# Kernel tuning notes

Measured on AMD Instinct MI355X. Metric: run time of the kernel, lower is better.

Reference implementation:

```python
import jax, jax.numpy as jnp
import numpy as np

V_EN = 50000; V_FR = 50000; D = 256; B = 64; S = 64; NEG = 8192; PAD = 0


def setup_inputs() -> dict:
    key = jax.random.key(0)
    k = jax.random.split(key, 8)
    zs = jax.random.normal(k[0], (B, S, D), dtype=jnp.float32) * 0.1
    x_en = jax.random.randint(k[1], (B, S), 1, V_EN)  # avoid pad row 0
    x_fr = jax.random.randint(k[2], (B, S), 1, V_FR)
    en_mask = jnp.ones((B, S), dtype=jnp.float32)
    fr_mask = jnp.ones((B, S), dtype=jnp.float32)
    W_en = jax.random.normal(k[3], (V_EN, D), dtype=jnp.float32) * 0.05
    W_en = W_en.at[PAD].set(0.0)  # padding_idx row is zero
    W_fr = jax.random.normal(k[4], (V_FR, D), dtype=jnp.float32) * 0.05
    W_fr = W_fr.at[PAD].set(0.0)
    # Host-side CSS sampling, mirroring the torch module's numpy/multinomial step.
    rng = np.random.default_rng(0)
    pos_en = np.unique(np.asarray(x_en))
    neg_en = rng.choice(np.setdiff1d(np.arange(V_EN), pos_en), NEG, replace=False)
    kappa_en = jnp.float32((V_EN - pos_en.shape[0]) / NEG)
    pos_fr = np.unique(np.asarray(x_fr))
    neg_fr = rng.choice(np.setdiff1d(np.arange(V_FR), pos_fr), NEG, replace=False)
    kappa_fr = jnp.float32((V_FR - pos_fr.shape[0]) / NEG)
    return {
        "zs": zs, "x_en": x_en, "x_fr": x_fr,
        "en_mask": en_mask, "fr_mask": fr_mask,
        "W_en": W_en, "W_fr": W_fr,
        "pos_en": jnp.asarray(pos_en), "neg_en": jnp.asarray(neg_en),
        "pos_fr": jnp.asarray(pos_fr), "neg_fr": jnp.asarray(neg_fr),
        "kappa_en": kappa_en, "kappa_fr": kappa_fr,
    }


def _css_denom(zs, W, pos_idx, neg_idx, kappa):
    # zs: [B,S,D]; pos/neg embeddings: [P,D]/[N,D] -> denom [B,S]
    pos_e = W[pos_idx]
    neg_e = W[neg_idx]
    pos_score = jnp.exp(jnp.einsum("bsd,pd->bsp", zs, pos_e)).sum(-1)
    neg_score = kappa * jnp.exp(jnp.einsum("bsd,nd->bsn", zs, neg_e)).sum(-1)
    return pos_score + neg_score


def reference(zs, x_en, x_fr, en_mask, fr_mask, W_en, W_fr,
              pos_en, neg_en, pos_fr, neg_fr, kappa_en, kappa_fr):
    # --- English CSS: per-token score ---
    be_en = W_en[x_en]                                   # [B,S,D]
    en_batch = jnp.exp((zs * be_en).sum(-1))             # [B,S]
    en_probs = en_batch / _css_denom(zs, W_en, pos_en, neg_en, kappa_en)
    # --- French CSS: alignment score against every en position ---
    be_fr = W_fr[x_fr]                                   # [B,Sf,D]
    fr_batch = jnp.exp(jnp.einsum("bfd,bsd->bfs", be_fr, zs))  # [B,Sf,S]
    fr_denom = _css_denom(zs, W_fr, pos_fr, neg_fr, kappa_fr)  # [B,S]
    fr_probs = fr_batch / fr_denom[:, None, :]
    en_rec_loss = (jnp.log(en_probs) * en_mask).sum(axis=1)            # [B]
    fr_rec_loss = (jnp.log(fr_probs.sum(axis=2)) * fr_mask).sum(axis=1)  # [B]
    return en_rec_loss, fr_rec_loss
```

## Files before the change

### kernel.cpp

```cpp
#include <hip/hip_runtime.h>

#define DDIM 256
#define NTOK 4096
#define NEGN 8192
#define TM 64
#define TN 64
#define LDT 40

typedef __attribute__((ext_vector_type(8))) short bf16x8;
typedef __attribute__((ext_vector_type(4))) float f32x4;

__device__ inline unsigned short f2bf(float f) {
    unsigned int u = __float_as_uint(f);
    unsigned int r = u + 0x7FFFu + ((u >> 16) & 1u);
    return (unsigned short)(r >> 16);
}

__device__ inline void gl_lds16(const unsigned short* g, unsigned short* l) {
    __builtin_amdgcn_global_load_lds(
        reinterpret_cast<__attribute__((address_space(1))) unsigned int*>(
            reinterpret_cast<uintptr_t>(g)),
        reinterpret_cast<__attribute__((address_space(3))) unsigned int*>(
            reinterpret_cast<uintptr_t>(l)),
        16, 0, 0);
}

__device__ inline void wait_vmcnt2() { asm volatile("s_waitcnt vmcnt(2)" ::: "memory"); }
__device__ inline void wait_vmcnt1() { asm volatile("s_waitcnt vmcnt(1)" ::: "memory"); }
__device__ inline void wait_vmcnt0() { asm volatile("s_waitcnt vmcnt(0)" ::: "memory"); }
__device__ inline void raw_barrier() { asm volatile("s_barrier" ::: "memory"); }

template<int CTRL>
__device__ inline float dpp_add(float x) {
    int v = __builtin_amdgcn_update_dpp(0, __float_as_int(x), CTRL, 0xF, 0xF, false);
    return x + __int_as_float(v);
}
__device__ inline float red16(float x) {
    x = dpp_add<0xB1>(x);
    x = dpp_add<0x4E>(x);
    x = dpp_add<0x141>(x);
    x = dpp_add<0x140>(x);
    return x;
}

__global__ void gather_kernel(
    const float* __restrict__ zs,
    const float* __restrict__ W_en, const float* __restrict__ W_fr,
    const int* __restrict__ pos_en, const int* __restrict__ neg_en,
    const int* __restrict__ pos_fr, const int* __restrict__ neg_fr,
    const int* __restrict__ x_en,
    unsigned short* __restrict__ z_bf,
    unsigned short* __restrict__ E_en, unsigned short* __restrict__ E_fr,
    float* __restrict__ en_score,
    float* __restrict__ denom_en, float* __restrict__ denom_fr,
    int Pe, int Pf, int Lpe, int Lpf)
{
    int row  = blockIdx.x * 4 + (threadIdx.x >> 6);
    int lane = threadIdx.x & 63;
    const float* src = nullptr;
    unsigned short* dst = nullptr;
    bool zero = false;

    if (row < NTOK) {
        src = zs + (size_t)row * DDIM;
        dst = z_bf + (size_t)row * DDIM;
        if (lane == 0) { denom_en[row] = 0.0f; denom_fr[row] = 0.0f; }
    } else if (row < NTOK + Lpe) {
        int j = row - NTOK;
        int Le = Pe + NEGN;
        int idx = 0;
        if (j < Pe)      idx = pos_en[j];
        else if (j < Le) idx = neg_en[j - Pe];
        else             zero = true;
        src = W_en + (size_t)idx * DDIM;
        dst = E_en + (size_t)j * DDIM;
    } else if (row < NTOK + Lpe + Lpf) {
        int j = row - NTOK - Lpe;
        int Lf = Pf + NEGN;
        int idx = 0;
        if (j < Pf)      idx = pos_fr[j];
        else if (j < Lf) idx = neg_fr[j - Pf];
        else             zero = true;
        src = W_fr + (size_t)idx * DDIM;
        dst = E_fr + (size_t)j * DDIM;
    } else if (row < NTOK + Lpe + Lpf + NTOK) {
        int j = row - NTOK - Lpe - Lpf;
        int idx = x_en[j];
        float4 z = *(const float4*)(zs   + (size_t)j   * DDIM + lane * 4);
        float4 w = *(const float4*)(W_en + (size_t)idx * DDIM + lane * 4);
        float s = z.x * w.x + z.y * w.y + z.z * w.z + z.w * w.w;
        #pragma unroll
        for (int m = 32; m; m >>= 1) s += __shfl_xor(s, m);
        if (lane == 0) en_score[j] = s;
        return;
    } else {
        return;
    }

    int d = lane * 4;
    float4 v;
    if (zero) { v.x = v.y = v.z = v.w = 0.0f; }
    else      { v = *(const float4*)(src + d); }
    ushort4 o;
    o.x = f2bf(v.x); o.y = f2bf(v.y); o.z = f2bf(v.z); o.w = f2bf(v.w);
    *(ushort4*)(dst + d) = o;
}

__global__ __launch_bounds__(256, 2) void expsum_stream(
    const unsigned short* __restrict__ A,
    const unsigned short* __restrict__ E,
    const float* __restrict__ kep, const float* __restrict__ kfp,
    float* __restrict__ out_en, float* __restrict__ out_fr,
    int Pe, int Pf, int Lpe, int NT)
{
    __shared__ __align__(16) unsigned short Bs[4][2048];

    int lin = blockIdx.y * 64 + blockIdx.x;
    int xcd = lin & 7;
    int xb  = (lin >> 3) & 15;
    int sl  = xcd + 8 * (lin >> 7);

    int t    = threadIdx.x;
    int lane = t & 63;
    int wave = t >> 6;
    int col  = lane & 15;
    int quad = lane >> 4;

    float ke = kep[0], kf = kfp[0];
    asm volatile("" : "+v"(ke), "+v"(kf) : : "memory");

    bf16x8 afr[4][8];
    {
        const unsigned short* Ap =
            A + ((size_t)(xb * 256 + wave * 64 + col)) * DDIM + quad * 8;
        #pragma unroll
        for (int i = 0; i < 4; i++)
            #pragma unroll
            for (int c = 0; c < 8; c++)
                afr[i][c] = *(const bf16x8*)(Ap + (size_t)i * 16 * DDIM + c * 32);
    }

    float sums[4][4];
    #pragma unroll
    for (int i = 0; i < 4; i++)
        #pragma unroll
        for (int rr = 0; rr < 4; rr++) sums[i][rr] = 0.0f;
    float* curout = out_en;
    int outrow = xb * 256 + wave * 64;

    int ntiles = (NT - sl + 31) >> 5;
    int C = ntiles * 8;

    #define STAGE(c) do {                                                     \
        int tl_ = sl + (((c) >> 3) << 5);                                     \
        int kk_ = ((c) & 7) * 32;                                             \
        const unsigned short* g_ =                                            \
            E + (size_t)(tl_ * 64 + wave * 16 + col) * DDIM + kk_ + quad * 8; \
        gl_lds16(g_, &Bs[(c) & 3][wave * 512]);                               \
    } while (0)

    STAGE(0);
    STAGE(1);

    for (int s = 0; s < ntiles; s++) {
        int tl = sl + (s << 5);
        int nb = tl * 64;

        float* o = (nb >= Lpe) ? out_fr : out_en;
        if (o != curout) {
            #pragma unroll
            for (int i = 0; i < 4; i++)
                #pragma unroll
                for (int rr = 0; rr < 4; rr++) {
                    float v = red16(sums[i][rr]);
                    if (col == 0)
                        atomicAdd(curout + outrow + 16 * i + quad * 4 + rr, v);
                    sums[i][rr] = 0.0f;
                }
            curout = o;
        }

        float wj[4];
        #pragma unroll
        for (int j = 0; j < 4; j++) {
            int ngl = nb + 16 * j + col;
            if (nb < Lpe) {
                wj[j] = (ngl < Pe) ? 1.0f : ((ngl < Pe + NEGN) ? ke : 0.0f);
            } else {
                int nl = ngl - Lpe;
                wj[j] = (nl < Pf) ? 1.0f : ((nl < Pf + NEGN) ? kf : 0.0f);
            }
        }

        f32x4 acc[4][4];
        #pragma unroll
        for (int i = 0; i < 4; i++)
            #pragma unroll
            for (int j = 0; j < 4; j++)
                acc[i][j] = (f32x4){0.f, 0.f, 0.f, 0.f};

        #pragma unroll
        for (int k8 = 0; k8 < 8; k8++) {
            int c  = s * 8 + k8;
            int rb = c & 3;
            if (c + 2 < C) {
                STAGE(c + 2);
                wait_vmcnt2();
            } else if (c + 1 < C) {
                wait_vmcnt1();
            } else {
                wait_vmcnt0();
            }
            raw_barrier();

            bf16x8 bfv[4];
            #pragma unroll
            for (int j = 0; j < 4; j++)
                bfv[j] = *(const bf16x8*)(&Bs[rb][j * 512 + quad * 128 + col * 8]);
            #pragma unroll
            for (int j = 0; j < 4; j++)
                #pragma unroll
                for (int i = 0; i < 4; i++)
                    acc[i][j] = __builtin_amdgcn_mfma_f32_16x16x32_bf16(
                        afr[i][k8], bfv[j], acc[i][j], 0, 0, 0);
        }

        #pragma unroll
        for (int i = 0; i < 4; i++)
            #pragma unroll
            for (int rr = 0; rr < 4; rr++) {
                sums[i][rr] += wj[0] * __expf(acc[i][0][rr])
                             + wj[1] * __expf(acc[i][1][rr])
                             + wj[2] * __expf(acc[i][2][rr])
                             + wj[3] * __expf(acc[i][3][rr]);
            }
    }
    #undef STAGE

    #pragma unroll
    for (int i = 0; i < 4; i++)
        #pragma unroll
        for (int rr = 0; rr < 4; rr++) {
            float v = red16(sums[i][rr]);
            if (col == 0)
                atomicAdd(curout + outrow + 16 * i + quad * 4 + rr, v);
        }
}

__global__ __launch_bounds__(256) void expsum_gemm64_loss(
    const float* __restrict__ W_fr,
    const int* __restrict__ x_fr,
    const unsigned short* __restrict__ Bm,
    const float* __restrict__ denom_fr,
    const float* __restrict__ denom_en,
    const float* __restrict__ en_score,
    const float* __restrict__ en_mask,
    const float* __restrict__ fr_mask,
    float* __restrict__ outloss)
{
    __shared__ __align__(16) unsigned short lda[TM * LDT];
    __shared__ __align__(16) unsigned short ldb[TN * LDT];
    __shared__ float tbuf[64];

    int batch = blockIdx.x;
    const unsigned short* Bb = Bm + (size_t)batch * TN * DDIM;

    int t      = threadIdx.x;
    int srow   = t >> 2;
    int schunk = t & 3;
    int lane   = t & 63;
    int wave   = t >> 6;
    int col    = lane & 15;
    int quad   = lane >> 4;

    int aidx = x_fr[batch * 64 + srow];
    const float* Arow = W_fr + (size_t)aidx * DDIM;

    f32x4 acc0 = {0.f,0.f,0.f,0.f};
    f32x4 acc1 = {0.f,0.f,0.f,0.f};
    f32x4 acc2 = {0.f,0.f,0.f,0.f};
    f32x4 acc3 = {0.f,0.f,0.f,0.f};

    for (int kk = 0; kk < DDIM; kk += 32) {
        float4 f0 = *(const float4*)(Arow + kk + schunk * 8);
        float4 f1 = *(const float4*)(Arow + kk + schunk * 8 + 4);
        uint4 bv = *(const uint4*)(Bb + (size_t)srow * DDIM + kk + schunk * 8);
        ushort4 ua; ua.x = f2bf(f0.x); ua.y = f2bf(f0.y); ua.z = f2bf(f0.z); ua.w = f2bf(f0.w);
        ushort4 ub; ub.x = f2bf(f1.x); ub.y = f2bf(f1.y); ub.z = f2bf(f1.z); ub.w = f2bf(f1.w);
        __syncthreads();
        *(ushort4*)(lda + srow * LDT + schunk * 8)     = ua;
        *(ushort4*)(lda + srow * LDT + schunk * 8 + 4) = ub;
        *(uint4*)(ldb + srow * LDT + schunk * 8) = bv;
        __syncthreads();

        bf16x8 af = *(const bf16x8*)(lda + (wave * 16 + col) * LDT + quad * 8);
        bf16x8 b0 = *(const bf16x8*)(ldb + ( 0 + col) * LDT + quad * 8);
        bf16x8 b1 = *(const bf16x8*)(ldb + (16 + col) * LDT + quad * 8);
        bf16x8 b2 = *(const bf16x8*)(ldb + (32 + col) * LDT + quad * 8);
        bf16x8 b3 = *(const bf16x8*)(ldb + (48 + col) * LDT + quad * 8);
        acc0 = __builtin_amdgcn_mfma_f32_16x16x32_bf16(af, b0, acc0, 0, 0, 0);
        acc1 = __builtin_amdgcn_mfma_f32_16x16x32_bf16(af, b1, acc1, 0, 0, 0);
        acc2 = __builtin_amdgcn_mfma_f32_16x16x32_bf16(af, b2, acc2, 0, 0, 0);
        acc3 = __builtin_amdgcn_mfma_f32_16x16x32_bf16(af, b3, acc3, 0, 0, 0);
    }

    const float* db = denom_fr + batch * 64;
    float w0 = 1.0f / db[ 0 + col];
    float w1 = 1.0f / db[16 + col];
    float w2 = 1.0f / db[32 + col];
    float w3 = 1.0f / db[48 + col];

    float tot0 = w0 * __expf(acc0.x) + w1 * __expf(acc1.x) + w2 * __expf(acc2.x) + w3 * __expf(acc3.x);
    float tot1 = w0 * __expf(acc0.y) + w1 * __expf(acc1.y) + w2 * __expf(acc2.y) + w3 * __expf(acc3.y);
    float tot2 = w0 * __expf(acc0.z) + w1 * __expf(acc1.z) + w2 * __expf(acc2.z) + w3 * __expf(acc3.z);
    float tot3 = w0 * __expf(acc0.w) + w1 * __expf(acc1.w) + w2 * __expf(acc2.w) + w3 * __expf(acc3.w);

    #pragma unroll
    for (int m = 1; m < 16; m <<= 1) {
        tot0 += __shfl_xor(tot0, m);
        tot1 += __shfl_xor(tot1, m);
        tot2 += __shfl_xor(tot2, m);
        tot3 += __shfl_xor(tot3, m);
    }
    if (col == 0) {
        int base = wave * 16 + quad * 4;
        tbuf[base + 0] = tot0; tbuf[base + 1] = tot1;
        tbuf[base + 2] = tot2; tbuf[base + 3] = tot3;
    }
    __syncthreads();

    if (t < 64) {
        int i = batch * 64 + t;
        float a = (en_score[i] - __logf(denom_en[i])) * en_mask[i];
        float c = __logf(tbuf[t]) * fr_mask[i];
        #pragma unroll
        for (int m = 32; m; m >>= 1) { a += __shfl_xor(a, m); c += __shfl_xor(c, m); }
        if (t == 0) { outloss[batch] = a; outloss[64 + batch] = c; }
    }
}

extern "C" void kernel_launch(void* const* d_in, const int* in_sizes, int n_in,
                              void* d_out, int out_size, void* d_ws, size_t ws_size,
                              hipStream_t stream)
{
    const float* zs       = (const float*)d_in[0];
    const int*   x_en     = (const int*)d_in[1];
    const int*   x_fr     = (const int*)d_in[2];
    const float* en_mask  = (const float*)d_in[3];
    const float* fr_mask  = (const float*)d_in[4];
    const float* W_en     = (const float*)d_in[5];
    const float* W_fr     = (const float*)d_in[6];
    const int*   pos_en   = (const int*)d_in[7];
    const int*   neg_en   = (const int*)d_in[8];
    const int*   pos_fr   = (const int*)d_in[9];
    const int*   neg_fr   = (const int*)d_in[10];
    const float* kappa_en = (const float*)d_in[11];
    const float* kappa_fr = (const float*)d_in[12];

    int Pe  = in_sizes[7];
    int Pf  = in_sizes[9];
    int Lpe = (Pe + NEGN + 63) & ~63;
    int Lpf = (Pf + NEGN + 63) & ~63;
    int Ltot = Lpe + Lpf;
    int NT   = Ltot / 64;

    char* w = (char*)d_ws;
    float* denom_en = (float*)w; w += NTOK * 4;
    float* denom_fr = (float*)w; w += NTOK * 4;
    float* en_score = (float*)w; w += NTOK * 4;
    unsigned short* z_bf  = (unsigned short*)w; w += (size_t)NTOK * DDIM * 2;
    unsigned short* E_all = (unsigned short*)w; w += (size_t)Ltot * DDIM * 2;

    int totrows = NTOK + Lpe + Lpf + NTOK;
    gather_kernel<<<(totrows + 3) / 4, 256, 0, stream>>>(
        zs, W_en, W_fr, pos_en, neg_en, pos_fr, neg_fr, x_en,
        z_bf, E_all, E_all + (size_t)Lpe * DDIM,
        en_score, denom_en, denom_fr, Pe, Pf, Lpe, Lpf);

    expsum_stream<<<dim3(64, 8), 256, 0, stream>>>(
        z_bf, E_all, kappa_en, kappa_fr, denom_en, denom_fr, Pe, Pf, Lpe, NT);

    expsum_gemm64_loss<<<64, 256, 0, stream>>>(
        W_fr, x_fr, z_bf, denom_fr, denom_en, en_score, en_mask, fr_mask,
        (float*)d_out);
}
```

Before: 202.2 us.

## Split expsum stream into single-wave blocks with barrier-free triple-buffered prefetch

The streaming exp-sum GEMM now runs as 2048 blocks of one 64-lane wave, where it used to be 512 blocks of four waves sharing each LDS tile. Each wave loads the full 64-row embedding tile into LDS on its own, so the workgroup s_barrier is gone. Prefetch depth rises from two to three stages, with vmcnt waits adjusted to match. The cost is that waves no longer share E tiles, so each tile is fetched once per 64-row token group rather than once per 256-row group, roughly quadrupling L2/LDS fill traffic for E.

```diff
diff --git a/kernel.cpp b/kernel.cpp
--- a/kernel.cpp
+++ b/kernel.cpp
@@ -25,10 +25,9 @@
         16, 0, 0);
 }
 
-__device__ inline void wait_vmcnt2() { asm volatile("s_waitcnt vmcnt(2)" ::: "memory"); }
-__device__ inline void wait_vmcnt1() { asm volatile("s_waitcnt vmcnt(1)" ::: "memory"); }
+__device__ inline void wait_vmcnt8() { asm volatile("s_waitcnt vmcnt(8)" ::: "memory"); }
+__device__ inline void wait_vmcnt4() { asm volatile("s_waitcnt vmcnt(4)" ::: "memory"); }
 __device__ inline void wait_vmcnt0() { asm volatile("s_waitcnt vmcnt(0)" ::: "memory"); }
-__device__ inline void raw_barrier() { asm volatile("s_barrier" ::: "memory"); }
 
 template<int CTRL>
 __device__ inline float dpp_add(float x) {
@@ -106,7 +105,7 @@
     *(ushort4*)(dst + d) = o;
 }
 
-__global__ __launch_bounds__(256, 2) void expsum_stream(
+__global__ __launch_bounds__(64, 2) void expsum_stream(
     const unsigned short* __restrict__ A,
     const unsigned short* __restrict__ E,
     const float* __restrict__ kep, const float* __restrict__ kfp,
@@ -115,14 +114,12 @@
 {
     __shared__ __align__(16) unsigned short Bs[4][2048];
 
-    int lin = blockIdx.y * 64 + blockIdx.x;
+    int lin = blockIdx.x;
     int xcd = lin & 7;
-    int xb  = (lin >> 3) & 15;
-    int sl  = xcd + 8 * (lin >> 7);
-
-    int t    = threadIdx.x;
-    int lane = t & 63;
-    int wave = t >> 6;
+    int sl  = xcd + 8 * ((lin >> 3) & 3);
+    int mg  = lin >> 5;
+
+    int lane = threadIdx.x;
     int col  = lane & 15;
     int quad = lane >> 4;
 
@@ -131,8 +128,7 @@
 
     bf16x8 afr[4][8];
     {
-        const unsigned short* Ap =
-            A + ((size_t)(xb * 256 + wave * 64 + col)) * DDIM + quad * 8;
+        const unsigned short* Ap = A + ((size_t)(mg * 64 + col)) * DDIM + quad * 8;
         #pragma unroll
         for (int i = 0; i < 4; i++)
             #pragma unroll
@@ -146,7 +142,7 @@
         #pragma unroll
         for (int rr = 0; rr < 4; rr++) sums[i][rr] = 0.0f;
     float* curout = out_en;
-    int outrow = xb * 256 + wave * 64;
+    int outrow = mg * 64;
 
     int ntiles = (NT - sl + 31) >> 5;
     int C = ntiles * 8;
@@ -155,12 +151,17 @@
         int tl_ = sl + (((c) >> 3) << 5);                                     \
         int kk_ = ((c) & 7) * 32;                                             \
         const unsigned short* g_ =                                            \
-            E + (size_t)(tl_ * 64 + wave * 16 + col) * DDIM + kk_ + quad * 8; \
-        gl_lds16(g_, &Bs[(c) & 3][wave * 512]);                               \
+            E + (size_t)(tl_ * 64 + col) * DDIM + kk_ + quad * 8;             \
+        unsigned short* l_ = &Bs[(c) & 3][0];                                 \
+        gl_lds16(g_,             l_);                                         \
+        gl_lds16(g_ + 16 * DDIM, l_ + 512);                                   \
+        gl_lds16(g_ + 32 * DDIM, l_ + 1024);                                  \
+        gl_lds16(g_ + 48 * DDIM, l_ + 1536);                                  \
     } while (0)
 
     STAGE(0);
     STAGE(1);
+    STAGE(2);
 
     for (int s = 0; s < ntiles; s++) {
         int tl = sl + (s << 5);
@@ -201,22 +202,22 @@
 
         #pragma unroll
         for (int k8 = 0; k8 < 8; k8++) {
-            int c  = s * 8 + k8;
-            int rb = c & 3;
+            int c = s * 8 + k8;
             if (c + 2 < C) {
-                STAGE(c + 2);
-                wait_vmcnt2();
+                wait_vmcnt8();
             } else if (c + 1 < C) {
-                wait_vmcnt1();
+                wait_vmcnt4();
             } else {
                 wait_vmcnt0();
             }
-            raw_barrier();
 
             bf16x8 bfv[4];
             #pragma unroll
             for (int j = 0; j < 4; j++)
-                bfv[j] = *(const bf16x8*)(&Bs[rb][j * 512 + quad * 128 + col * 8]);
+                bfv[j] = *(const bf16x8*)(&Bs[c & 3][j * 512 + quad * 128 + col * 8]);
+
+            if (c + 3 < C) STAGE(c + 3);
+
             #pragma unroll
             for (int j = 0; j < 4; j++)
                 #pragma unroll
@@ -377,7 +378,7 @@
         z_bf, E_all, E_all + (size_t)Lpe * DDIM,
         en_score, denom_en, denom_fr, Pe, Pf, Lpe, Lpf);
 
-    expsum_stream<<<dim3(64, 8), 256, 0, stream>>>(
+    expsum_stream<<<2048, 64, 0, stream>>>(
         z_bf, E_all, kappa_en, kappa_fr, denom_en, denom_fr, Pe, Pf, Lpe, NT);
 
     expsum_gemm64_loss<<<64, 256, 0, stream>>>(
```

Result: slower. 246.5 us (+21.9%).

## Double-buffer whole E tiles in LDS with one barrier per tile

Applied to the files above, without the earlier changes.

Replaces the per-k-chunk four-slot ring buffer with a two-tile double buffer that prefetches all eight k-chunks of the next tile at once. Each tile now needs a single wait and barrier instead of eight, cutting synchronisation overhead and lengthening the prefetch distance. LDS use per block grows fourfold, which could limit occupancy. The full drain at the start of each tile may expose memory latency if the previous tile's compute does not cover it.

```diff
diff --git a/kernel.cpp b/kernel.cpp
--- a/kernel.cpp
+++ b/kernel.cpp
@@ -25,8 +25,6 @@
         16, 0, 0);
 }
 
-__device__ inline void wait_vmcnt2() { asm volatile("s_waitcnt vmcnt(2)" ::: "memory"); }
-__device__ inline void wait_vmcnt1() { asm volatile("s_waitcnt vmcnt(1)" ::: "memory"); }
 __device__ inline void wait_vmcnt0() { asm volatile("s_waitcnt vmcnt(0)" ::: "memory"); }
 __device__ inline void raw_barrier() { asm volatile("s_barrier" ::: "memory"); }
 
@@ -113,7 +111,7 @@
     float* __restrict__ out_en, float* __restrict__ out_fr,
     int Pe, int Pf, int Lpe, int NT)
 {
-    __shared__ __align__(16) unsigned short Bs[4][2048];
+    __shared__ __align__(16) unsigned short Bs[2][8][2048];
 
     int lin = blockIdx.y * 64 + blockIdx.x;
     int xcd = lin & 7;
@@ -149,22 +147,27 @@
     int outrow = xb * 256 + wave * 64;
 
     int ntiles = (NT - sl + 31) >> 5;
-    int C = ntiles * 8;
-
-    #define STAGE(c) do {                                                     \
-        int tl_ = sl + (((c) >> 3) << 5);                                     \
-        int kk_ = ((c) & 7) * 32;                                             \
-        const unsigned short* g_ =                                            \
-            E + (size_t)(tl_ * 64 + wave * 16 + col) * DDIM + kk_ + quad * 8; \
-        gl_lds16(g_, &Bs[(c) & 3][wave * 512]);                               \
+
+    #define STAGE_TILE(s) do {                                               \
+        int tl_ = sl + ((s) << 5);                                           \
+        const unsigned short* g_ =                                           \
+            E + (size_t)(tl_ * 64 + wave * 16 + col) * DDIM + quad * 8;      \
+        unsigned short* l_ = &Bs[(s) & 1][0][wave * 512];                    \
+        _Pragma("unroll")                                                    \
+        for (int kc_ = 0; kc_ < 8; kc_++)                                    \
+            gl_lds16(g_ + kc_ * 32, l_ + kc_ * 2048);                        \
     } while (0)
 
-    STAGE(0);
-    STAGE(1);
+    STAGE_TILE(0);
 
     for (int s = 0; s < ntiles; s++) {
         int tl = sl + (s << 5);
         int nb = tl * 64;
+
+        wait_vmcnt0();
+        raw_barrier();
+
+        if (s + 1 < ntiles) STAGE_TILE(s + 1);
 
         float* o = (nb >= Lpe) ? out_fr : out_en;
         if (o != curout) {
@@ -201,22 +204,11 @@
 
         #pragma unroll
         for (int k8 = 0; k8 < 8; k8++) {
-            int c  = s * 8 + k8;
-            int rb = c & 3;
-            if (c + 2 < C) {
-                STAGE(c + 2);
-                wait_vmcnt2();
-            } else if (c + 1 < C) {
-                wait_vmcnt1();
-            } else {
-                wait_vmcnt0();
-            }
-            raw_barrier();
-
             bf16x8 bfv[4];
             #pragma unroll
             for (int j = 0; j < 4; j++)
-                bfv[j] = *(const bf16x8*)(&Bs[rb][j * 512 + quad * 128 + col * 8]);
+                bfv[j] = *(const bf16x8*)(
+                    &Bs[s & 1][k8][j * 512 + quad * 128 + col * 8]);
             #pragma unroll
             for (int j = 0; j < 4; j++)
                 #pragma unroll
@@ -235,7 +227,7 @@
                              + wj[3] * __expf(acc[i][3][rr]);
             }
     }
-    #undef STAGE
+    #undef STAGE_TILE
 
     #pragma unroll
     for (int i = 0; i < 4; i++)
```

Result: faster. 198.1 us (-2.0%).
